# Kernel optimization log

Hardware: AMD Instinct MI355X
Metric: run time of the kernel (lower is better)

Reference implementation:

```python
import jax, jax.numpy as jnp
import numpy as np

ALPHA = 0.2  # LeakyReLU slope
NEG_BIG = -9e15


def setup_inputs() -> dict:
    key = jax.random.key(0)
    ks = jax.random.split(key, 6)
    N, F_IN, F_OUT, F_E = 8192, 256, 64, 8
    h = jax.random.normal(ks[0], (N, F_IN), dtype=jnp.float32)
    edge = jax.random.normal(ks[1], (N, F_E), dtype=jnp.float32)
    adj = jax.random.randint(ks[2], (N, N), 0, 2, dtype=jnp.int32)
    W = jax.random.normal(ks[3], (F_IN, F_OUT), dtype=jnp.float32) * 0.09  # ~xavier
    a = jax.random.normal(ks[4], (3 * F_OUT, 1), dtype=jnp.float32) * 0.12
    We = jax.random.normal(ks[5], (F_E, F_OUT), dtype=jnp.float32) * 0.28
    return {"h": h, "edge": edge, "adj": adj, "W": W, "a": a, "We": We}


def reference(h, edge, adj, W, a, We):
    F_OUT = W.shape[1]
    Wh = h @ W                      # [N, F]
    WeE = edge @ We                 # [N, F]
    a1 = a[:F_OUT, 0]               # source term
    a2 = a[F_OUT:2 * F_OUT, 0]      # target term
    a3 = a[2 * F_OUT:, 0]           # edge (source-indexed) term
    # e[i, j] = leakyrelu(Wh[i].a1 + Wh[j].a2 + WeE[i].a3)  == original repeat/cat @ a
    src = Wh @ a1 + WeE @ a3        # [N]
    dst = Wh @ a2                   # [N]
    e = jax.nn.leaky_relu(src[:, None] + dst[None, :], negative_slope=ALPHA)
    scores = jnp.where(adj > 0, e, NEG_BIG)
    attention = jax.nn.softmax(scores, axis=1)  # dropout p=0.0 / eval: identity
    h_prime = attention @ Wh        # [N, F]
    return jax.nn.elu(h_prime)      # concat=True
```

## Files before the change

### kernel.cpp

```cpp
#include <hip/hip_runtime.h>

typedef float v4f __attribute__((ext_vector_type(4)));
typedef short v8s __attribute__((ext_vector_type(8)));

#define ALPHA 0.2f
#define LOG2E 1.44269504088896340736f
#define NROW 8192
#define FIN 256
#define FOUT 64
#define JSPLIT 8
#define JCHUNK (NROW / JSPLIT)
#define NSTEP (JCHUNK / 32)

static __device__ __forceinline__ unsigned short f2bf(float f) {
  unsigned int u = __builtin_bit_cast(unsigned int, f);
  u += 0x7fff + ((u >> 16) & 1);
  return (unsigned short)(u >> 16);
}
static __device__ __forceinline__ float bf2f(unsigned short s) {
  unsigned int u = ((unsigned int)s) << 16;
  return __builtin_bit_cast(float, u);
}

__global__ __launch_bounds__(256) void k1_proj(
    const float* __restrict__ h, const float* __restrict__ edge,
    const float* __restrict__ W, const float* __restrict__ a,
    const float* __restrict__ We, unsigned short* __restrict__ whT,
    float* __restrict__ srcv, float* __restrict__ dstv) {
  __shared__ float Ws[FIN * FOUT];
  int tid = threadIdx.x;
  const float4* Wg = (const float4*)W;
  float4* Wl = (float4*)Ws;
#pragma unroll
  for (int it = 0; it < 16; ++it) Wl[it * 256 + tid] = Wg[it * 256 + tid];
  int lane = tid & 63;
  int wave = tid >> 6;
  float a1c = a[lane], a2c = a[64 + lane], a3c = a[128 + lane];
  float Wer[8];
#pragma unroll
  for (int k = 0; k < 8; ++k) Wer[k] = We[k * 64 + lane];
  __syncthreads();
  int rbase = blockIdx.x * 16 + wave * 4;
  for (int rr = 0; rr < 4; ++rr) {
    int r = rbase + rr;
    const float* hr = h + r * FIN;
    float acc = 0.f;
#pragma unroll 4
    for (int k = 0; k < FIN; k += 4) {
      float4 hv = *(const float4*)(hr + k);
      acc += hv.x * Ws[(k + 0) * 64 + lane];
      acc += hv.y * Ws[(k + 1) * 64 + lane];
      acc += hv.z * Ws[(k + 2) * 64 + lane];
      acc += hv.w * Ws[(k + 3) * 64 + lane];
    }
    float4 e0 = *(const float4*)(edge + r * 8);
    float4 e1 = *(const float4*)(edge + r * 8 + 4);
    float acc2 = e0.x * Wer[0] + e0.y * Wer[1] + e0.z * Wer[2] + e0.w * Wer[3] +
                 e1.x * Wer[4] + e1.y * Wer[5] + e1.z * Wer[6] + e1.w * Wer[7];
    float ps = acc * a1c + acc2 * a3c;
    float pd = acc * a2c;
#pragma unroll
    for (int off = 32; off >= 1; off >>= 1) {
      ps += __shfl_xor(ps, off);
      pd += __shfl_xor(pd, off);
    }
    whT[lane * NROW + r] = f2bf(acc);
    if (lane == 0) {
      srcv[r] = ps;
      dstv[r] = pd;
    }
  }
}

__global__ __launch_bounds__(256) void k1b_dstmax(const float* __restrict__ dstv,
                                                  float* __restrict__ dmax) {
  int tid = threadIdx.x;
  float m = -1e30f;
  for (int k = tid; k < NROW; k += 256) m = fmaxf(m, dstv[k]);
#pragma unroll
  for (int off = 32; off >= 1; off >>= 1) m = fmaxf(m, __shfl_xor(m, off));
  __shared__ float red[4];
  if ((tid & 63) == 0) red[tid >> 6] = m;
  __syncthreads();
  if (tid == 0) dmax[0] = fmaxf(fmaxf(red[0], red[1]), fmaxf(red[2], red[3]));
}

struct Buf {
  int4 aj0, aj1;
  float4 d0, d1;
  v8s b0, b1, b2, b3;
};

static __device__ __forceinline__ void loadstep(
    Buf& B, const int* __restrict__ adj, const float* __restrict__ dstv,
    const unsigned short* __restrict__ whT, int row, int g, int m, int jj) {
  const int* ap = adj + (long)row * NROW + jj + g * 8;
  B.aj0 = *(const int4*)ap;
  B.aj1 = *(const int4*)(ap + 4);
  const float* dp = dstv + jj + g * 8;
  B.d0 = *(const float4*)dp;
  B.d1 = *(const float4*)(dp + 4);
  const unsigned short* wp = whT + jj + g * 8;
  B.b0 = *(const v8s*)(wp + (m + 0) * NROW);
  B.b1 = *(const v8s*)(wp + (m + 16) * NROW);
  B.b2 = *(const v8s*)(wp + (m + 32) * NROW);
  B.b3 = *(const v8s*)(wp + (m + 48) * NROW);
}

static __device__ __forceinline__ void computestep(const Buf& B, float sv,
                                                   float M2, v4f& a0, v4f& a1,
                                                   v4f& a2, v4f& a3,
                                                   float& ssum) {
  v8s aw;
#define WCALC(adji, dsti, slot)                                 \
  {                                                             \
    float x = sv + (dsti);                                      \
    float lr = fmaxf(x, ALPHA * x);                             \
    float w = exp2f(__builtin_fmaf(lr, LOG2E, -M2));            \
    unsigned short wb = ((adji) > 0) ? f2bf(w) : (unsigned short)0; \
    ssum += bf2f(wb);                                           \
    aw[slot] = (short)wb;                                       \
  }
  WCALC(B.aj0.x, B.d0.x, 0)
  WCALC(B.aj0.y, B.d0.y, 1)
  WCALC(B.aj0.z, B.d0.z, 2)
  WCALC(B.aj0.w, B.d0.w, 3)
  WCALC(B.aj1.x, B.d1.x, 4)
  WCALC(B.aj1.y, B.d1.y, 5)
  WCALC(B.aj1.z, B.d1.z, 6)
  WCALC(B.aj1.w, B.d1.w, 7)
#undef WCALC
  a0 = __builtin_amdgcn_mfma_f32_16x16x32_bf16(aw, B.b0, a0, 0, 0, 0);
  a1 = __builtin_amdgcn_mfma_f32_16x16x32_bf16(aw, B.b1, a1, 0, 0, 0);
  a2 = __builtin_amdgcn_mfma_f32_16x16x32_bf16(aw, B.b2, a2, 0, 0, 0);
  a3 = __builtin_amdgcn_mfma_f32_16x16x32_bf16(aw, B.b3, a3, 0, 0, 0);
}

__global__ __launch_bounds__(256) void k2_attn(
    const int* __restrict__ adj, const float* __restrict__ srcg,
    const float* __restrict__ dstv, const float* __restrict__ dmax,
    const unsigned short* __restrict__ whT, float* __restrict__ hpart,
    float* __restrict__ spart) {
  int tid = threadIdx.x;
  int lane = tid & 63;
  int wave = tid >> 6;
  int rtile = blockIdx.x * 64 + wave * 16;
  int jy = blockIdx.y;
  int jbase = jy * JCHUNK;
  int m = lane & 15;
  int g = lane >> 4;
  int row = rtile + m;
  float sv = srcg[row];
  float dm = dmax[0];
  float xm = sv + dm;
  float M2 = fmaxf(xm, ALPHA * xm) * LOG2E;
  v4f a0 = {}, a1 = {}, a2 = {}, a3 = {};
  float ssum = 0.f;
  Buf BA, BB;
  loadstep(BA, adj, dstv, whT, row, g, m, jbase);
  for (int t = 0; t < NSTEP; t += 2) {
    loadstep(BB, adj, dstv, whT, row, g, m, jbase + (t + 1) * 32);
    computestep(BA, sv, M2, a0, a1, a2, a3, ssum);
    if (t + 2 < NSTEP)
      loadstep(BA, adj, dstv, whT, row, g, m, jbase + (t + 2) * 32);
    computestep(BB, sv, M2, a0, a1, a2, a3, ssum);
  }
  ssum += __shfl_xor(ssum, 16);
  ssum += __shfl_xor(ssum, 32);
  if (g == 0) spart[jy * NROW + row] = ssum;
  float* hp = hpart + ((long)jy * NROW + rtile) * FOUT;
#pragma unroll
  for (int r = 0; r < 4; ++r) {
    hp[(g * 4 + r) * FOUT + 0 + m] = a0[r];
    hp[(g * 4 + r) * FOUT + 16 + m] = a1[r];
    hp[(g * 4 + r) * FOUT + 32 + m] = a2[r];
    hp[(g * 4 + r) * FOUT + 48 + m] = a3[r];
  }
}

__global__ __launch_bounds__(256) void k3_fin(const float* __restrict__ hpart,
                                              const float* __restrict__ spart,
                                              float* __restrict__ out) {
  long gid = (long)blockIdx.x * 256 + threadIdx.x;
  int i = (int)(gid >> 6);
  float num = 0.f, den = 0.f;
#pragma unroll
  for (int p = 0; p < JSPLIT; ++p) {
    num += hpart[(long)p * NROW * FOUT + gid];
    den += spart[p * NROW + i];
  }
  float v = num / den;
  out[gid] = v > 0.f ? v : (__expf(v) - 1.0f);
}

extern "C" void kernel_launch(void* const* d_in, const int* in_sizes, int n_in,
                              void* d_out, int out_size, void* d_ws,
                              size_t ws_size, hipStream_t stream) {
  const float* h = (const float*)d_in[0];
  const float* edge = (const float*)d_in[1];
  const int* adj = (const int*)d_in[2];
  const float* W = (const float*)d_in[3];
  const float* a = (const float*)d_in[4];
  const float* We = (const float*)d_in[5];
  float* out = (float*)d_out;
  char* ws = (char*)d_ws;
  unsigned short* whT = (unsigned short*)ws;
  float* srcv = (float*)(ws + 1048576);
  float* dstv = (float*)(ws + 1081344);
  float* dmax = (float*)(ws + 1114112);
  float* spart = (float*)(ws + 1114368);
  float* hpart = (float*)(ws + 1376512);
  hipLaunchKernelGGL(k1_proj, dim3(512), dim3(256), 0, stream, h, edge, W, a,
                     We, whT, srcv, dstv);
  hipLaunchKernelGGL(k1b_dstmax, dim3(1), dim3(256), 0, stream, dstv, dmax);
  hipLaunchKernelGGL(k2_attn, dim3(128, JSPLIT), dim3(256), 0, stream, adj,
                     srcv, dstv, dmax, whT, hpart, spart);
  hipLaunchKernelGGL(k3_fin, dim3(2048), dim3(256), 0, stream, hpart, spart,
                     out);
}
```

Before: 461.9 us.

## Tile bf16 Wh transpose into 32-row blocks and register-block projection rows

Stores the transposed bf16 Wh in 32-column tiles so each MFMA B-operand load in the attention kernel reads a contiguous 4KB block instead of striding by the full row length. This is meant to improve cache-line locality for the B-operand loads. The projection kernel also computes four rows at once, sharing each shared-memory W read across the four rows. The cost is more live registers in the projection kernel, and both kernels now depend on the new tiled index formula.

```diff
diff --git a/kernel.cpp b/kernel.cpp
--- a/kernel.cpp
+++ b/kernel.cpp
@@ -41,30 +41,47 @@
   for (int k = 0; k < 8; ++k) Wer[k] = We[k * 64 + lane];
   __syncthreads();
   int rbase = blockIdx.x * 16 + wave * 4;
+  const float* hr0 = h + (long)(rbase + 0) * FIN;
+  const float* hr1 = h + (long)(rbase + 1) * FIN;
+  const float* hr2 = h + (long)(rbase + 2) * FIN;
+  const float* hr3 = h + (long)(rbase + 3) * FIN;
+  float acc0 = 0.f, acc1 = 0.f, acc2 = 0.f, acc3 = 0.f;
+#pragma unroll 2
+  for (int k = 0; k < FIN; k += 4) {
+    float4 h0 = *(const float4*)(hr0 + k);
+    float4 h1 = *(const float4*)(hr1 + k);
+    float4 h2 = *(const float4*)(hr2 + k);
+    float4 h3 = *(const float4*)(hr3 + k);
+#pragma unroll
+    for (int t = 0; t < 4; ++t) {
+      float w = Ws[(k + t) * 64 + lane];
+      float e0 = (t == 0) ? h0.x : (t == 1) ? h0.y : (t == 2) ? h0.z : h0.w;
+      float e1 = (t == 0) ? h1.x : (t == 1) ? h1.y : (t == 2) ? h1.z : h1.w;
+      float e2 = (t == 0) ? h2.x : (t == 1) ? h2.y : (t == 2) ? h2.z : h2.w;
+      float e3 = (t == 0) ? h3.x : (t == 1) ? h3.y : (t == 2) ? h3.z : h3.w;
+      acc0 = __builtin_fmaf(e0, w, acc0);
+      acc1 = __builtin_fmaf(e1, w, acc1);
+      acc2 = __builtin_fmaf(e2, w, acc2);
+      acc3 = __builtin_fmaf(e3, w, acc3);
+    }
+  }
+#pragma unroll
   for (int rr = 0; rr < 4; ++rr) {
     int r = rbase + rr;
-    const float* hr = h + r * FIN;
-    float acc = 0.f;
-#pragma unroll 4
-    for (int k = 0; k < FIN; k += 4) {
-      float4 hv = *(const float4*)(hr + k);
-      acc += hv.x * Ws[(k + 0) * 64 + lane];
-      acc += hv.y * Ws[(k + 1) * 64 + lane];
-      acc += hv.z * Ws[(k + 2) * 64 + lane];
-      acc += hv.w * Ws[(k + 3) * 64 + lane];
-    }
+    float acc = (rr == 0) ? acc0 : (rr == 1) ? acc1 : (rr == 2) ? acc2 : acc3;
     float4 e0 = *(const float4*)(edge + r * 8);
     float4 e1 = *(const float4*)(edge + r * 8 + 4);
-    float acc2 = e0.x * Wer[0] + e0.y * Wer[1] + e0.z * Wer[2] + e0.w * Wer[3] +
-                 e1.x * Wer[4] + e1.y * Wer[5] + e1.z * Wer[6] + e1.w * Wer[7];
-    float ps = acc * a1c + acc2 * a3c;
+    float aedge = e0.x * Wer[0] + e0.y * Wer[1] + e0.z * Wer[2] +
+                  e0.w * Wer[3] + e1.x * Wer[4] + e1.y * Wer[5] +
+                  e1.z * Wer[6] + e1.w * Wer[7];
+    float ps = acc * a1c + aedge * a3c;
     float pd = acc * a2c;
 #pragma unroll
     for (int off = 32; off >= 1; off >>= 1) {
       ps += __shfl_xor(ps, off);
       pd += __shfl_xor(pd, off);
     }
-    whT[lane * NROW + r] = f2bf(acc);
+    whT[((long)(r >> 5)) * 2048 + lane * 32 + (r & 31)] = f2bf(acc);
     if (lane == 0) {
       srcv[r] = ps;
       dstv[r] = pd;
@@ -100,11 +117,11 @@
   const float* dp = dstv + jj + g * 8;
   B.d0 = *(const float4*)dp;
   B.d1 = *(const float4*)(dp + 4);
-  const unsigned short* wp = whT + jj + g * 8;
-  B.b0 = *(const v8s*)(wp + (m + 0) * NROW);
-  B.b1 = *(const v8s*)(wp + (m + 16) * NROW);
-  B.b2 = *(const v8s*)(wp + (m + 32) * NROW);
-  B.b3 = *(const v8s*)(wp + (m + 48) * NROW);
+  const unsigned short* wp = whT + ((long)(jj >> 5)) * 2048 + m * 32 + g * 8;
+  B.b0 = *(const v8s*)(wp + 0);
+  B.b1 = *(const v8s*)(wp + 512);
+  B.b2 = *(const v8s*)(wp + 1024);
+  B.b3 = *(const v8s*)(wp + 1536);
 }
 
 static __device__ __forceinline__ void computestep(const Buf& B, float sv,
```

Result: faster. 440.5 us (-4.6%).
